# Optimization experiments

Measured on AMD Instinct MI355X. Metric: run time of the kernel, lower is better.

Reference implementation:

```python
import jax, jax.numpy as jnp
import numpy as np

T = 64        # n_estimators
DEPTH = 8
D = 2**DEPTH - 1   # internal nodes per tree (255)
K = 2**DEPTH       # leaves per tree (256)
M = 512       # n_features
C = 8         # class_num
B = 4096      # batch


def _build_path_masks():
    # Complete binary tree in heap order. For leaf l, walk from root;
    # going LEFT corresponds to b==+1 -> multiply (1 - x_node) -> Bpos,
    # going RIGHT corresponds to b==-1 -> multiply x_node -> Bneg.
    Bpos = np.zeros((K, D), dtype=np.float32)
    Bneg = np.zeros((K, D), dtype=np.float32)
    for l in range(K):
        node = 0
        for level in range(DEPTH):
            bit = (l >> (DEPTH - 1 - level)) & 1
            if bit == 0:
                Bpos[l, node] = 1.0
            else:
                Bneg[l, node] = 1.0
            node = 2 * node + 1 + bit
    return Bpos, Bneg


def setup_inputs() -> dict:
    rng = np.random.default_rng(0)
    key = jax.random.key(0)
    x = jax.random.normal(key, (B, M), dtype=jnp.float32)
    # fcn1: each internal node splits on one feature -> one-hot weight row,
    # bias = -threshold (change_parameters1).
    feat = rng.integers(0, M, size=(T, D))
    W1 = np.zeros((T, D, M), dtype=np.float32)
    W1[np.arange(T)[:, None], np.arange(D)[None, :], feat] = 1.0
    b1 = (-rng.standard_normal((T, D))).astype(np.float32)  # -threshold
    # Path masks shared across trees (complete trees), tiled per tree.
    Bpos1, Bneg1 = _build_path_masks()
    Bpos = np.broadcast_to(Bpos1, (T, K, D)).copy()
    Bneg = np.broadcast_to(Bneg1, (T, K, D)).copy()
    # fcn2 weight = c^T with zero bias (change_parameters2): leaf values [T, K, C]
    Cw = rng.random((T, K, C)).astype(np.float32)
    return {
        "input": x,
        "W1": jnp.asarray(W1),
        "b1": jnp.asarray(b1),
        "Bpos": jnp.asarray(Bpos),
        "Bneg": jnp.asarray(Bneg),
        "Cw": jnp.asarray(Cw),
    }


def reference(input, W1, b1, Bpos, Bneg, Cw):
    # z: [B, T, D] = 10 * (fcn1 per tree)
    z = 10.0 * (jnp.einsum("bm,tdm->btd", input, W1) + b1)
    # x = sigmoid(z); leaf-path product:
    #   x_c[b,t,k] = prod_d x^Bneg[t,k,d] * (1-x)^Bpos[t,k,d]
    # computed exactly in log-space (all factors in (0,1)):
    log_x = jax.nn.log_sigmoid(z)       # log sigmoid(z)
    log_1mx = jax.nn.log_sigmoid(-z)    # log (1 - sigmoid(z))
    log_xc = (jnp.einsum("btd,tkd->btk", log_x, Bneg)
              + jnp.einsum("btd,tkd->btk", log_1mx, Bpos))
    x_c = jnp.exp(log_xc)               # [B, T, K]
    # fcn2 (zero bias) then forest average over trees
    out = jnp.einsum("btk,tkc->bc", x_c, Cw) / T
    return out
```

## Files before the change

kernel.cpp:

```cpp
#include <hip/hip_runtime.h>
#include <hip/hip_bf16.h>

#define TT 64
#define DD 255
#define KK 256
#define MM 512
#define CC 8
#define BB 4096
#define RB 16
#define TPB 16
#define ST 18

typedef _Float16 h8 __attribute__((ext_vector_type(8)));
typedef _Float16 h2v __attribute__((ext_vector_type(2)));
typedef float f4 __attribute__((ext_vector_type(4)));

__device__ __forceinline__ h2v pkrtz(float a, float b) {
    return __builtin_bit_cast(h2v, __builtin_amdgcn_cvt_pkrtz(a, b));
}

__device__ __forceinline__ float wave_sum(float v) {
    v += __shfl_down(v, 32, 64);
    v += __shfl_down(v, 16, 64);
    v += __shfl_down(v, 8, 64);
    v += __shfl_down(v, 4, 64);
    v += __shfl_down(v, 2, 64);
    v += __shfl_down(v, 1, 64);
    return v;
}

__global__ void feat_kernel(const float* __restrict__ W1, int* __restrict__ feat) {
    const int row = blockIdx.x * 4 + (threadIdx.x >> 6);
    const int lane = threadIdx.x & 63;
    const float4* r = reinterpret_cast<const float4*>(W1 + (size_t)row * MM);
    float4 a = r[lane];
    float4 b = r[lane + 64];
    float ba = (float)(4 * lane);
    float bb = (float)(4 * (lane + 64));
    float acc = 0.0f;
    acc = fmaf(a.x, ba,        acc);
    acc = fmaf(a.y, ba + 1.0f, acc);
    acc = fmaf(a.z, ba + 2.0f, acc);
    acc = fmaf(a.w, ba + 3.0f, acc);
    acc = fmaf(b.x, bb,        acc);
    acc = fmaf(b.y, bb + 1.0f, acc);
    acc = fmaf(b.z, bb + 2.0f, acc);
    acc = fmaf(b.w, bb + 3.0f, acc);
    acc = wave_sum(acc);
    if (lane == 0) feat[row] = (int)(acc + 0.5f);
}

__device__ __forceinline__ float sigm_from(float xv, float c1) {
    float earg = fmaf(-14.426950408889634f, xv, c1);
    float e = exp2f(earg);
    return __builtin_amdgcn_rcpf(1.0f + e);
}

__global__ __launch_bounds__(256, 2) void forest_kernel(
        const float* __restrict__ x, const float* __restrict__ b1,
        const float* __restrict__ Cw, const int* __restrict__ feat,
        float* __restrict__ out) {
    __shared__ _Float16 xsi[MM * ST];
    __shared__ _Float16 s8[4][256 * ST];
    __shared__ __align__(16) _Float16 cwl[4][8 * 8 * 5 * 8];
    __shared__ f4 red[4][64];

    const int tid = threadIdx.x;
    const int w = tid >> 6;
    const int lane = tid & 63;
    const int b0 = blockIdx.x * RB;
    const int t0 = blockIdx.y * TPB;
    const int m = lane & 15;
    const int slot = lane >> 4;

    for (int idx = tid; idx < MM * RB; idx += 256) {
        int mm = idx & (MM - 1);
        int r = idx >> 9;
        xsi[mm * ST + r] = (_Float16)x[(size_t)(b0 + r) * MM + mm];
    }
    __syncthreads();

    _Float16* s8w = s8[w];
    _Float16* cww = cwl[w];

    const int b3 = slot >> 1, b4 = slot & 1;
    const float sg3 = (float)(2 * b3 - 1), off3 = (float)(1 - b3);
    const float sg4 = (float)(2 * b4 - 1), off4 = (float)(1 - b4);

    f4 acc = {0.f, 0.f, 0.f, 0.f};

    for (int tt = 0; tt < 4; ++tt) {
        const int t = t0 + w * 4 + tt;
        asm volatile("" ::: "memory");

        #pragma unroll
        for (int kq = 0; kq < 4; ++kq) {
            int d = kq * 64 + lane;
            if (d < DD) {
                int f = feat[t * DD + d];
                float c1 = -14.426950408889634f * b1[t * DD + d];
                const uint32_t* xp = reinterpret_cast<const uint32_t*>(xsi + f * ST);
                uint32_t* sp = reinterpret_cast<uint32_t*>(s8w + d * ST);
                #pragma unroll
                for (int i2 = 0; i2 < 8; ++i2) {
                    h2v u = __builtin_bit_cast(h2v, xp[i2]);
                    float sa = sigm_from((float)u.x, c1);
                    float sb = sigm_from((float)u.y, c1);
                    sp[i2] = __builtin_bit_cast(uint32_t, pkrtz(sa, sb));
                }
            }
        }

        #pragma unroll
        for (int kq = 0; kq < 4; ++kq) {
            int k = kq * 64 + lane;
            const float4* cp = reinterpret_cast<const float4*>(Cw + ((size_t)t * KK + k) * CC);
            float4 p0 = cp[0], p1 = cp[1];
            int cc = k >> 5, sl = (k >> 3) & 3, j = k & 7;
            _Float16* bp = cww + cc * 320 + sl * 8 + j;
            bp[0 * 40] = (_Float16)p0.x;
            bp[1 * 40] = (_Float16)p0.y;
            bp[2 * 40] = (_Float16)p0.z;
            bp[3 * 40] = (_Float16)p0.w;
            bp[4 * 40] = (_Float16)p1.x;
            bp[5 * 40] = (_Float16)p1.y;
            bp[6 * 40] = (_Float16)p1.z;
            bp[7 * 40] = (_Float16)p1.w;
        }
        asm volatile("s_waitcnt lgkmcnt(0)" ::: "memory");

        float s0 = (float)s8w[0 * ST + m];
        float s1 = (float)s8w[1 * ST + m];
        float s2 = (float)s8w[2 * ST + m];
        float s3 = (float)s8w[3 * ST + m];
        float s4 = (float)s8w[4 * ST + m];
        float s5p = (float)s8w[5 * ST + m];
        float s6 = (float)s8w[6 * ST + m];
        float P10 = 1.0f - s0, P11 = s0;
        float P200 = P10 * (1.0f - s1), P201 = P10 * s1;
        float P210 = P11 * (1.0f - s2), P211 = P11 * s2;
        float P3a[8];
        P3a[0] = P200 * (1.0f - s3); P3a[1] = P200 * s3;
        P3a[2] = P201 * (1.0f - s4); P3a[3] = P201 * s4;
        P3a[4] = P210 * (1.0f - s5p); P3a[5] = P210 * s5p;
        P3a[6] = P211 * (1.0f - s6); P3a[7] = P211 * s6;

        #pragma unroll
        for (int c = 0; c < 8; ++c) {
            const int n3 = 7 + c;
            float sc3 = (float)s8w[n3 * ST + m];
            float f3 = fmaf(sg3, sc3, off3);
            int n4 = 2 * n3 + 1 + b3;
            float sc4 = (float)s8w[n4 * ST + m];
            float f4v = fmaf(sg4, sc4, off4);
            float P5 = P3a[c] * f3 * f4v;
            int n5 = 2 * n4 + 1 + b4;
            float s5 = (float)s8w[n5 * ST + m];
            float v1 = P5 * s5, v0 = P5 - v1;
            int q0 = 2 * n5 + 1;
            float sq0 = (float)s8w[q0 * ST + m];
            float sq1 = (float)s8w[(q0 + 1) * ST + m];
            float w01 = v0 * sq0, w00 = v0 - w01;
            float w11 = v1 * sq1, w10 = v1 - w11;
            int r0 = 2 * q0 + 1;
            float sr0 = (float)s8w[(r0 + 0) * ST + m];
            float sr1 = (float)s8w[(r0 + 1) * ST + m];
            float sr2 = (float)s8w[(r0 + 2) * ST + m];
            float sr3 = (float)s8w[(r0 + 3) * ST + m];
            float l1 = w00 * sr0, l0 = w00 - l1;
            float l3 = w01 * sr1, l2 = w01 - l3;
            float l5 = w10 * sr2, l4 = w10 - l5;
            float l7 = w11 * sr3, l6 = w11 - l7;
            union { h8 v; h2v p[4]; } U;
            U.p[0] = pkrtz(l0, l1);
            U.p[1] = pkrtz(l2, l3);
            U.p[2] = pkrtz(l4, l5);
            U.p[3] = pkrtz(l6, l7);
            h8 bf = {};
            if (m < CC)
                bf = *reinterpret_cast<const h8*>(cww + (c * 8 + m) * 40 + slot * 8);
            acc = __builtin_amdgcn_mfma_f32_16x16x32_f16(U.v, bf, acc, 0, 0, 0);
        }
    }

    red[w][lane] = acc;
    __syncthreads();
    if (tid < 64) {
        f4 sum = red[0][tid];
        sum += red[1][tid];
        sum += red[2][tid];
        sum += red[3][tid];
        int n = tid & 15, sl = tid >> 4;
        if (n < CC) {
            #pragma unroll
            for (int reg = 0; reg < 4; ++reg) {
                int row = sl * 4 + reg;
                atomicAdd(&out[(size_t)(b0 + row) * CC + n], sum[reg] * (1.0f / 64.0f));
            }
        }
    }
}

extern "C" void kernel_launch(void* const* d_in, const int* in_sizes, int n_in,
                              void* d_out, int out_size, void* d_ws, size_t ws_size,
                              hipStream_t stream) {
    const float* x  = (const float*)d_in[0];
    const float* W1 = (const float*)d_in[1];
    const float* b1 = (const float*)d_in[2];
    const float* Cw = (const float*)d_in[5];
    float* out = (float*)d_out;
    int* feat = (int*)d_ws;

    (void)hipMemsetAsync(out, 0, (size_t)BB * CC * sizeof(float), stream);
    feat_kernel<<<(TT * DD) / 4, 256, 0, stream>>>(W1, feat);
    forest_kernel<<<dim3(BB / RB, TT / TPB), 256, 0, stream>>>(x, b1, Cw, feat, out);
}
```

Measured before the change: 147.7 us.

## Pretranspose leaf values to fp16 once and load MFMA B-operands directly

A new cwt_kernel converts Cw to fp16 once, in the MFMA B-operand layout, stored in the workspace. The forest kernel then loads its B fragments straight into registers instead of having every block convert and scatter Cw into LDS for each tree. The x staging layout in LDS is also compacted (row stride of 17 halves, with odd features sharing a row) and reused as the reduction buffer, which cuts LDS use and may raise occupancy. The costs are an extra small launch and eight h8 registers per thread held for the B fragments.

Measured after the change: 147.4 us. About the same (-0.2%).

```diff
diff --git a/kernel.cpp b/kernel.cpp
--- a/kernel.cpp
+++ b/kernel.cpp
@@ -50,6 +50,23 @@
     if (lane == 0) feat[row] = (int)(acc + 0.5f);
 }
 
+__global__ void cwt_kernel(const float* __restrict__ Cw, _Float16* __restrict__ cwT) {
+    int idx = blockIdx.x * 256 + threadIdx.x;
+    int t = idx >> 8, k = idx & 255;
+    int c = k >> 5, sl = (k >> 3) & 3, j = k & 7;
+    const float4* p = reinterpret_cast<const float4*>(Cw + (size_t)idx * CC);
+    float4 p0 = p[0], p1 = p[1];
+    _Float16* base = cwT + ((((t * 8 + c) * 8) * 4 + sl) * 8 + j);
+    base[0 * 32] = (_Float16)p0.x;
+    base[1 * 32] = (_Float16)p0.y;
+    base[2 * 32] = (_Float16)p0.z;
+    base[3 * 32] = (_Float16)p0.w;
+    base[4 * 32] = (_Float16)p1.x;
+    base[5 * 32] = (_Float16)p1.y;
+    base[6 * 32] = (_Float16)p1.z;
+    base[7 * 32] = (_Float16)p1.w;
+}
+
 __device__ __forceinline__ float sigm_from(float xv, float c1) {
     float earg = fmaf(-14.426950408889634f, xv, c1);
     float e = exp2f(earg);
@@ -58,12 +75,10 @@
 
 __global__ __launch_bounds__(256, 2) void forest_kernel(
         const float* __restrict__ x, const float* __restrict__ b1,
-        const float* __restrict__ Cw, const int* __restrict__ feat,
+        const _Float16* __restrict__ cwT, const int* __restrict__ feat,
         float* __restrict__ out) {
-    __shared__ _Float16 xsi[MM * ST];
+    __shared__ __align__(16) _Float16 xsi[(MM / 2) * 34];
     __shared__ _Float16 s8[4][256 * ST];
-    __shared__ __align__(16) _Float16 cwl[4][8 * 8 * 5 * 8];
-    __shared__ f4 red[4][64];
 
     const int tid = threadIdx.x;
     const int w = tid >> 6;
@@ -76,12 +91,11 @@
     for (int idx = tid; idx < MM * RB; idx += 256) {
         int mm = idx & (MM - 1);
         int r = idx >> 9;
-        xsi[mm * ST + r] = (_Float16)x[(size_t)(b0 + r) * MM + mm];
+        xsi[17 * mm - (mm & 1) + r] = (_Float16)x[(size_t)(b0 + r) * MM + mm];
     }
     __syncthreads();
 
     _Float16* s8w = s8[w];
-    _Float16* cww = cwl[w];
 
     const int b3 = slot >> 1, b4 = slot & 1;
     const float sg3 = (float)(2 * b3 - 1), off3 = (float)(1 - b3);
@@ -99,7 +113,7 @@
             if (d < DD) {
                 int f = feat[t * DD + d];
                 float c1 = -14.426950408889634f * b1[t * DD + d];
-                const uint32_t* xp = reinterpret_cast<const uint32_t*>(xsi + f * ST);
+                const uint32_t* xp = reinterpret_cast<const uint32_t*>(xsi) + ((17 * f) >> 1);
                 uint32_t* sp = reinterpret_cast<uint32_t*>(s8w + d * ST);
                 #pragma unroll
                 for (int i2 = 0; i2 < 8; ++i2) {
@@ -111,21 +125,12 @@
             }
         }
 
-        #pragma unroll
-        for (int kq = 0; kq < 4; ++kq) {
-            int k = kq * 64 + lane;
-            const float4* cp = reinterpret_cast<const float4*>(Cw + ((size_t)t * KK + k) * CC);
-            float4 p0 = cp[0], p1 = cp[1];
-            int cc = k >> 5, sl = (k >> 3) & 3, j = k & 7;
-            _Float16* bp = cww + cc * 320 + sl * 8 + j;
-            bp[0 * 40] = (_Float16)p0.x;
-            bp[1 * 40] = (_Float16)p0.y;
-            bp[2 * 40] = (_Float16)p0.z;
-            bp[3 * 40] = (_Float16)p0.w;
-            bp[4 * 40] = (_Float16)p1.x;
-            bp[5 * 40] = (_Float16)p1.y;
-            bp[6 * 40] = (_Float16)p1.z;
-            bp[7 * 40] = (_Float16)p1.w;
+        h8 bfr[8] = {};
+        if (m < CC) {
+            const h8* cp = reinterpret_cast<const h8*>(cwT) +
+                           (((t * 8 + 0) * 8 + m) * 4 + slot);
+            #pragma unroll
+            for (int c = 0; c < 8; ++c) bfr[c] = cp[c * 32];
         }
         asm volatile("s_waitcnt lgkmcnt(0)" ::: "memory");
 
@@ -176,20 +181,19 @@
             U.p[1] = pkrtz(l2, l3);
             U.p[2] = pkrtz(l4, l5);
             U.p[3] = pkrtz(l6, l7);
-            h8 bf = {};
-            if (m < CC)
-                bf = *reinterpret_cast<const h8*>(cww + (c * 8 + m) * 40 + slot * 8);
-            acc = __builtin_amdgcn_mfma_f32_16x16x32_f16(U.v, bf, acc, 0, 0, 0);
+            acc = __builtin_amdgcn_mfma_f32_16x16x32_f16(U.v, bfr[c], acc, 0, 0, 0);
         }
     }
 
-    red[w][lane] = acc;
+    __syncthreads();
+    f4* red = reinterpret_cast<f4*>(xsi);
+    red[w * 64 + lane] = acc;
     __syncthreads();
     if (tid < 64) {
-        f4 sum = red[0][tid];
-        sum += red[1][tid];
-        sum += red[2][tid];
-        sum += red[3][tid];
+        f4 sum = red[0 * 64 + tid];
+        sum += red[1 * 64 + tid];
+        sum += red[2 * 64 + tid];
+        sum += red[3 * 64 + tid];
         int n = tid & 15, sl = tid >> 4;
         if (n < CC) {
             #pragma unroll
@@ -209,9 +213,12 @@
     const float* b1 = (const float*)d_in[2];
     const float* Cw = (const float*)d_in[5];
     float* out = (float*)d_out;
-    int* feat = (int*)d_ws;
+
+    _Float16* cwT = (_Float16*)d_ws;
+    int* feat = (int*)((char*)d_ws + (size_t)TT * KK * CC * sizeof(_Float16));
 
     (void)hipMemsetAsync(out, 0, (size_t)BB * CC * sizeof(float), stream);
     feat_kernel<<<(TT * DD) / 4, 256, 0, stream>>>(W1, feat);
-    forest_kernel<<<dim3(BB / RB, TT / TPB), 256, 0, stream>>>(x, b1, Cw, feat, out);
-}
+    cwt_kernel<<<(TT * KK) / 256, 256, 0, stream>>>(Cw, cwT);
+    forest_kernel<<<dim3(BB / RB, TT / TPB), 256, 0, stream>>>(x, b1, cwT, feat, out);
+}
```
